# Kernel optimization log

Hardware: AMD Instinct MI355X
Metric: run time of the kernel (lower is better)

Reference implementation:

```python
import jax, jax.numpy as jnp
import numpy as np

B, T, D_IN = 512, 128, 256
H1, H2 = 1024, 1024
LABEL_DIM = 3


def _lstm_layer(x, W, U, b):
    """Run one keras-LSTMCell layer over x: [T, B, D_in] -> [T, B, H].

    Keras gate order is (i, f, g, o); c' = f*c + i*tanh(g); h = o*tanh(c').
    """
    H = U.shape[0]
    batch = x.shape[1]

    def step(carry, xt):
        h, c = carry
        z = xt @ W + h @ U + b  # [B, 4H]
        i, f, g, o = jnp.split(z, 4, axis=-1)
        i = jax.nn.sigmoid(i)
        f = jax.nn.sigmoid(f)
        g = jnp.tanh(g)
        o = jax.nn.sigmoid(o)
        c_new = f * c + i * g
        h_new = o * jnp.tanh(c_new)
        return (h_new, c_new), h_new

    init = (jnp.zeros((batch, H), x.dtype), jnp.zeros((batch, H), x.dtype))
    _, hs = jax.lax.scan(step, init, x)
    return hs  # [T, B, H]


def setup_inputs() -> dict:
    key = jax.random.key(0)
    ks = jax.random.split(key, 10)
    chars = jax.random.normal(ks[0], (B, T, D_IN), dtype=jnp.float32)
    # sequence lengths in [1, T] so sequence_length - 1 is a valid index
    sequence_length = jax.random.randint(ks[1], (B,), 1, T + 1)
    s = 0.05
    W1 = jax.random.normal(ks[2], (D_IN, 4 * H1), dtype=jnp.float32) * s
    U1 = jax.random.normal(ks[3], (H1, 4 * H1), dtype=jnp.float32) * s
    b1 = jnp.zeros((4 * H1,), dtype=jnp.float32)
    W2 = jax.random.normal(ks[4], (H1, 4 * H2), dtype=jnp.float32) * s
    U2 = jax.random.normal(ks[5], (H2, 4 * H2), dtype=jnp.float32) * s
    b2 = jnp.zeros((4 * H2,), dtype=jnp.float32)
    Wd = jax.random.normal(ks[6], (H2, LABEL_DIM), dtype=jnp.float32) * s
    bd = jnp.zeros((LABEL_DIM,), dtype=jnp.float32)
    return {"chars": chars, "sequence_length": sequence_length,
            "W1": W1, "U1": U1, "b1": b1,
            "W2": W2, "U2": U2, "b2": b2,
            "Wd": Wd, "bd": bd}


def reference(chars, sequence_length, W1, U1, b1, W2, U2, b2, Wd, bd):
    # chars: [B, T, 256] -> time-major [T, B, 256]
    x = jnp.transpose(chars, (1, 0, 2))
    x = _lstm_layer(x, W1, U1, b1)          # [T, B, H1]
    x = _lstm_layer(x, W2, U2, b2)          # [T, B, H2]
    # gather the hidden state at the last valid timestep of each sequence
    batch = chars.shape[0]
    hidden = x[sequence_length - 1, jnp.arange(batch)]  # [B, H2]
    return jax.nn.relu(hidden @ Wd + bd)    # [B, label_dim]
```

## Files before the change

### kernel.cpp

```cpp
#include <hip/hip_runtime.h>
#include <hip/hip_bf16.h>


typedef __hip_bfloat16 bf16;
typedef __attribute__((ext_vector_type(8))) short bfrag8;
typedef __attribute__((ext_vector_type(4))) float accf4;

#define BATCH 512
#define TSTEPS 128
#define DIN 256
#define H 1024
#define NG 4096

__device__ __forceinline__ float sigm(float x) { return 1.0f / (1.0f + __expf(-x)); }
__device__ __forceinline__ float tanh_f(float x) {
    float a = fabsf(x);
    float e = __expf(-2.0f * a);
    float t = (1.0f - e) / (1.0f + e);
    return x < 0.0f ? -t : t;
}
__device__ __forceinline__ unsigned short bfr16(float x) {
    bf16 h = __float2bfloat16(x);
    return *(unsigned short*)&h;
}
__device__ __forceinline__ void gll16(const void* g, void* l) {
    __builtin_amdgcn_global_load_lds(
        (const __attribute__((address_space(1))) unsigned int*)g,
        (__attribute__((address_space(3))) unsigned int*)l, 16, 0, 0);
}

__global__ void k_repack(const float* __restrict__ W, const float* __restrict__ U,
                         bf16* __restrict__ Bp, int KIN)
{
    __shared__ float tile[128][65];
    int kt = blockIdx.x, nt = blockIdx.y;
    int lane = threadIdx.x;
    int n = nt * 64 + lane;
    int orig = ((n >> 4) & 3) * 1024 + (n >> 7) * 32 + ((n >> 6) & 1) * 16 + (n & 15);
    for (int j = 0; j < 128; ++j) {
        int k = kt * 128 + j;
        tile[j][lane] = (k < KIN) ? W[(size_t)k * NG + orig]
                                  : U[(size_t)(k - KIN) * NG + orig];
    }
    __syncthreads();
    for (int u = 0; u < 16; ++u) {
        int cid = u * 64 + lane;
        int nloc = cid >> 4;
        int pos = cid & 15;
        int nn = nt * 64 + nloc;
        int kc = pos ^ (nn & 7);
        alignas(16) unsigned short pk[8];
        #pragma unroll
        for (int jj = 0; jj < 8; ++jj) pk[jj] = bfr16(tile[kc * 8 + jj][nloc]);
        *(int4*)(Bp + ((size_t)kt * NG + nn) * 128 + pos * 8) = *(int4*)pk;
    }
}

struct StepJob {
    const float* Xf;
    const bf16* A0;
    const bf16* A1;
    const bf16* Bp;
    const float* bias;
    float* C;
    bf16* Hout;
    float* hidden;
    const int* seqlen;
    int xstride;
    int ksplit;
    int KT;
    int t;
};

__global__ __launch_bounds__(256, 2) void k_step(StepJob j0, StepJob j1)
{
    __shared__ __align__(16) bf16 Alds[64 * 128];
    __shared__ __align__(16) bf16 Blds[128 * 128];

    const StepJob jb = (blockIdx.x >> 8) ? j1 : j0;
    int bi = blockIdx.x & 255;
    int tid = threadIdx.x;
    int wv = tid >> 6, lane = tid & 63;
    int ntile = bi & 31;
    int b0 = (bi >> 5) * 64;
    int n0 = ntile * 128;
    int mw = (wv & 1) * 32;
    int nw = (wv >> 1) * 64;
    int c = lane & 15, q = lane >> 4;

    const accf4 zero4 = {0.f, 0.f, 0.f, 0.f};
    accf4 acc[2][4];
    #pragma unroll
    for (int i = 0; i < 2; ++i)
        #pragma unroll
        for (int j = 0; j < 4; ++j) acc[i][j] = zero4;

    for (int kt = 0; kt < jb.KT; ++kt) {
        int k0 = kt << 7;
        if (jb.Xf && k0 < jb.ksplit) {
            #pragma unroll
            for (int uu = 0; uu < 4; ++uu) {
                int u = uu * 256 + tid;
                int r = u >> 4;
                int pos = u & 15;
                int kc = pos ^ (r & 7);
                const float* src = jb.Xf + (size_t)(b0 + r) * jb.xstride + k0 + kc * 8;
                float4 va = *(const float4*)src;
                float4 vb = *(const float4*)(src + 4);
                alignas(16) unsigned short pk[8];
                pk[0] = bfr16(va.x); pk[1] = bfr16(va.y);
                pk[2] = bfr16(va.z); pk[3] = bfr16(va.w);
                pk[4] = bfr16(vb.x); pk[5] = bfr16(vb.y);
                pk[6] = bfr16(vb.z); pk[7] = bfr16(vb.w);
                *(int4*)((char*)Alds + u * 16) = *(int4*)pk;
            }
        } else {
            const bf16* Asrc; int kk0;
            if (k0 < jb.ksplit) { Asrc = jb.A0; kk0 = k0; }
            else                { Asrc = jb.A1; kk0 = k0 - jb.ksplit; }
            #pragma unroll
            for (int cc = 0; cc < 4; ++cc) {
                int ob = wv * 4096 + cc * 1024;
                int o = ob + lane * 16;
                int r = o >> 8;
                const char* g = (const char*)Asrc + (size_t)(b0 + r) * (H * 2) + kk0 * 2 + (o & 255);
                gll16(g, (char*)Alds + ob);
            }
        }
        const char* Bg = (const char*)jb.Bp + ((size_t)kt * NG + n0) * 256;
        #pragma unroll
        for (int cc = 0; cc < 8; ++cc) {
            int ob = wv * 8192 + cc * 1024;
            gll16(Bg + ob + lane * 16, (char*)Blds + ob);
        }
        __syncthreads();
        #pragma unroll
        for (int kk = 0; kk < 128; kk += 32) {
            int kc = (kk >> 3) + q;
            int ra = mw + c;
            int pa = (kc ^ (ra & 7)) << 3;
            bfrag8 af0 = *(const bfrag8*)(Alds + ra * 128 + pa);
            bfrag8 af1 = *(const bfrag8*)(Alds + (ra + 16) * 128 + pa);
            #pragma unroll
            for (int nt = 0; nt < 4; ++nt) {
                int nn = nw + nt * 16 + c;
                bfrag8 bfv = *(const bfrag8*)(Blds + nn * 128 + ((kc ^ (nn & 7)) << 3));
                acc[0][nt] = __builtin_amdgcn_mfma_f32_16x16x32_bf16(af0, bfv, acc[0][nt], 0, 0, 0);
                acc[1][nt] = __builtin_amdgcn_mfma_f32_16x16x32_bf16(af1, bfv, acc[1][nt], 0, 0, 0);
            }
        }
        __syncthreads();
    }

    int hcol = ntile * 32 + (wv >> 1) * 16 + c;
    float bi_ = jb.bias[hcol],         bf_ = jb.bias[H + hcol];
    float bg_ = jb.bias[2 * H + hcol], bo_ = jb.bias[3 * H + hcol];
    int seg = hcol & ~127;
    int kc_ = (hcol & 127) >> 3;
    int jl = hcol & 7;
    #pragma unroll
    for (int mt = 0; mt < 2; ++mt) {
        #pragma unroll
        for (int reg = 0; reg < 4; ++reg) {
            int b = b0 + mw + mt * 16 + q * 4 + reg;
            float ig = sigm(acc[mt][0][reg] + bi_);
            float fg = sigm(acc[mt][1][reg] + bf_);
            float gv = tanh_f(acc[mt][2][reg] + bg_);
            float og = sigm(acc[mt][3][reg] + bo_);
            size_t ci = (size_t)b * H + hcol;
            float cv = fg * jb.C[ci] + ig * gv;
            jb.C[ci] = cv;
            float h = og * tanh_f(cv);
            jb.Hout[(size_t)b * H + seg + ((kc_ ^ (b & 7)) << 3) + jl] = __float2bfloat16(h);
            if (jb.hidden) {
                if (jb.seqlen[b] - 1 == jb.t) jb.hidden[ci] = h;
            }
        }
    }
}

__global__ void k_final(const float* __restrict__ hidden, const float* __restrict__ Wd,
                        const float* __restrict__ bd, float* __restrict__ out)
{
    int b = blockIdx.x;
    int l = threadIdx.x;
    float p0 = 0.f, p1 = 0.f, p2 = 0.f;
    for (int jj = l; jj < H; jj += 64) {
        float hv = hidden[(size_t)b * H + jj];
        p0 += hv * Wd[jj * 3 + 0];
        p1 += hv * Wd[jj * 3 + 1];
        p2 += hv * Wd[jj * 3 + 2];
    }
    #pragma unroll
    for (int off = 32; off > 0; off >>= 1) {
        p0 += __shfl_down(p0, off);
        p1 += __shfl_down(p1, off);
        p2 += __shfl_down(p2, off);
    }
    if (l == 0) {
        out[b * 3 + 0] = fmaxf(p0 + bd[0], 0.f);
        out[b * 3 + 1] = fmaxf(p1 + bd[1], 0.f);
        out[b * 3 + 2] = fmaxf(p2 + bd[2], 0.f);
    }
}

extern "C" void kernel_launch(void* const* d_in, const int* in_sizes, int n_in,
                              void* d_out, int out_size, void* d_ws, size_t ws_size,
                              hipStream_t stream)
{
    const float* chars = (const float*)d_in[0];
    const int* seqlen  = (const int*)d_in[1];
    const float* W1 = (const float*)d_in[2];
    const float* U1 = (const float*)d_in[3];
    const float* b1 = (const float*)d_in[4];
    const float* W2 = (const float*)d_in[5];
    const float* U2 = (const float*)d_in[6];
    const float* b2 = (const float*)d_in[7];
    const float* Wd = (const float*)d_in[8];
    const float* bd = (const float*)d_in[9];
    float* out = (float*)d_out;

    char* ws = (char*)d_ws;
    size_t off = 0;
    bf16* Bp1 = (bf16*)(ws + off); off += (size_t)10 * NG * 128 * 2;
    bf16* Bp2 = (bf16*)(ws + off); off += (size_t)16 * NG * 128 * 2;
    bf16* h1  = (bf16*)(ws + off); off += (size_t)2 * BATCH * H * 2;
    bf16* h2  = (bf16*)(ws + off); off += (size_t)2 * BATCH * H * 2;
    float* c1 = (float*)(ws + off); off += (size_t)BATCH * H * 4;
    float* c2 = (float*)(ws + off); off += (size_t)BATCH * H * 4;
    float* hidden = (float*)(ws + off); off += (size_t)BATCH * H * 4;
    if (ws_size < off) return;

    hipMemsetAsync(h1, 0, (size_t)2 * BATCH * H * 2, stream);
    hipMemsetAsync(h2, 0, (size_t)2 * BATCH * H * 2, stream);
    hipMemsetAsync(c1, 0, (size_t)BATCH * H * 4, stream);
    hipMemsetAsync(c2, 0, (size_t)BATCH * H * 4, stream);

    k_repack<<<dim3(10, 64), 64, 0, stream>>>(W1, U1, Bp1, 256);
    k_repack<<<dim3(16, 64), 64, 0, stream>>>(W2, U2, Bp2, 1024);

    const size_t HS = (size_t)BATCH * H;

    auto mkL1 = [&](int s) {
        StepJob J;
        J.Xf = chars + (size_t)s * DIN;  J.xstride = TSTEPS * DIN;
        J.A0 = nullptr;
        J.A1 = h1 + (size_t)((s + 1) & 1) * HS;
        J.Bp = Bp1; J.bias = b1; J.C = c1;
        J.Hout = h1 + (size_t)(s & 1) * HS;
        J.hidden = nullptr; J.seqlen = nullptr;
        J.ksplit = 256; J.KT = 10; J.t = s;
        return J;
    };
    auto mkL2 = [&](int s) {
        StepJob J;
        J.Xf = nullptr; J.xstride = 0;
        J.A0 = h1 + (size_t)(s & 1) * HS;
        J.A1 = h2 + (size_t)((s + 1) & 1) * HS;
        J.Bp = Bp2; J.bias = b2; J.C = c2;
        J.Hout = h2 + (size_t)(s & 1) * HS;
        J.hidden = hidden; J.seqlen = seqlen;
        J.ksplit = 1024; J.KT = 16; J.t = s;
        return J;
    };

    StepJob first = mkL1(0);
    k_step<<<256, 256, 0, stream>>>(first, first);
    for (int t = 0; t < TSTEPS - 1; ++t) {
        k_step<<<512, 256, 0, stream>>>(mkL2(t), mkL1(t + 1));
    }
    StepJob last = mkL2(TSTEPS - 1);
    k_step<<<256, 256, 0, stream>>>(last, last);
    k_final<<<512, 64, 0, stream>>>(hidden, Wd, bd, out);
}
```

Before: 3.660 ms.

## Replace per-step launches with persistent kernel using per-row-group atomic counters

```diff
diff --git a/kernel.cpp b/kernel.cpp
--- a/kernel.cpp
+++ b/kernel.cpp
@@ -56,126 +56,164 @@
     }
 }
 
-struct StepJob {
-    const float* Xf;
-    const bf16* A0;
-    const bf16* A1;
-    const bf16* Bp;
-    const float* bias;
-    float* C;
-    bf16* Hout;
-    float* hidden;
-    const int* seqlen;
-    int xstride;
-    int ksplit;
-    int KT;
-    int t;
+struct PP {
+    const float* chars; const int* seqlen;
+    const bf16* Bp1; const bf16* Bp2;
+    const float* b1; const float* b2;
+    bf16* h1; bf16* h2; float* hidden;
+    int* cnt1; int* cnt2;
 };
 
-__global__ __launch_bounds__(256, 2) void k_step(StepJob j0, StepJob j1)
+__global__ __launch_bounds__(256, 2) void k_persist(PP P)
 {
     __shared__ __align__(16) bf16 Alds[64 * 128];
     __shared__ __align__(16) bf16 Blds[128 * 128];
 
-    const StepJob jb = (blockIdx.x >> 8) ? j1 : j0;
-    int bi = blockIdx.x & 255;
-    int tid = threadIdx.x;
-    int wv = tid >> 6, lane = tid & 63;
-    int ntile = bi & 31;
-    int b0 = (bi >> 5) * 64;
-    int n0 = ntile * 128;
-    int mw = (wv & 1) * 32;
-    int nw = (wv >> 1) * 64;
-    int c = lane & 15, q = lane >> 4;
-
-    const accf4 zero4 = {0.f, 0.f, 0.f, 0.f};
-    accf4 acc[2][4];
+    const int bid = blockIdx.x;
+    const int job = bid >> 8;
+    const int bi = bid & 255;
+    const int tid = threadIdx.x;
+    const int wv = tid >> 6, lane = tid & 63;
+    const int ntile = bi & 31, rg = bi >> 5;
+    const int b0 = rg * 64, n0 = ntile * 128;
+    const int mw = (wv & 1) * 32, nw = (wv >> 1) * 64;
+    const int c = lane & 15, q = lane >> 4;
+
+    const bf16* Bp = job ? P.Bp2 : P.Bp1;
+    const float* bias = job ? P.b2 : P.b1;
+    const int KT = job ? 16 : 10;
+    const int ksplit = job ? 1024 : 256;
+    const size_t HS = (size_t)BATCH * H;
+
+    const int hcol = ntile * 32 + (wv >> 1) * 16 + c;
+    const float bi_ = bias[hcol],         bf_ = bias[H + hcol];
+    const float bg_ = bias[2 * H + hcol], bo_ = bias[3 * H + hcol];
+    const int seg = hcol & ~127;
+    const int kc_ = (hcol & 127) >> 3;
+    const int jl = hcol & 7;
+    int houti[8]; int hidi[8]; int sl[8]; float cellv[8];
     #pragma unroll
-    for (int i = 0; i < 2; ++i)
-        #pragma unroll
-        for (int j = 0; j < 4; ++j) acc[i][j] = zero4;
-
-    for (int kt = 0; kt < jb.KT; ++kt) {
-        int k0 = kt << 7;
-        if (jb.Xf && k0 < jb.ksplit) {
-            #pragma unroll
-            for (int uu = 0; uu < 4; ++uu) {
-                int u = uu * 256 + tid;
-                int r = u >> 4;
-                int pos = u & 15;
-                int kc = pos ^ (r & 7);
-                const float* src = jb.Xf + (size_t)(b0 + r) * jb.xstride + k0 + kc * 8;
-                float4 va = *(const float4*)src;
-                float4 vb = *(const float4*)(src + 4);
-                alignas(16) unsigned short pk[8];
-                pk[0] = bfr16(va.x); pk[1] = bfr16(va.y);
-                pk[2] = bfr16(va.z); pk[3] = bfr16(va.w);
-                pk[4] = bfr16(vb.x); pk[5] = bfr16(vb.y);
-                pk[6] = bfr16(vb.z); pk[7] = bfr16(vb.w);
-                *(int4*)((char*)Alds + u * 16) = *(int4*)pk;
-            }
-        } else {
-            const bf16* Asrc; int kk0;
-            if (k0 < jb.ksplit) { Asrc = jb.A0; kk0 = k0; }
-            else                { Asrc = jb.A1; kk0 = k0 - jb.ksplit; }
-            #pragma unroll
-            for (int cc = 0; cc < 4; ++cc) {
-                int ob = wv * 4096 + cc * 1024;
-                int o = ob + lane * 16;
-                int r = o >> 8;
-                const char* g = (const char*)Asrc + (size_t)(b0 + r) * (H * 2) + kk0 * 2 + (o & 255);
-                gll16(g, (char*)Alds + ob);
-            }
-        }
-        const char* Bg = (const char*)jb.Bp + ((size_t)kt * NG + n0) * 256;
+    for (int u = 0; u < 8; ++u) {
+        int b = b0 + mw + (u >> 2) * 16 + q * 4 + (u & 3);
+        houti[u] = b * H + seg + (((kc_ ^ (b & 7))) << 3) + jl;
+        hidi[u] = b * H + hcol;
+        sl[u] = job ? (P.seqlen[b] - 1) : -1;
+        cellv[u] = 0.f;
+    }
+
+    int* cme = (job ? P.cnt2 : P.cnt1) + rg * 16;
+    int* cn1 = P.cnt1 + rg * 16;
+    int* cn2 = P.cnt2 + rg * 16;
+
+    auto stageChars = [&](int t_, int k0) {
+        #pragma unroll
+        for (int uu = 0; uu < 4; ++uu) {
+            int u = uu * 256 + tid;
+            int r = u >> 4;
+            int pos = u & 15;
+            int kc = pos ^ (r & 7);
+            const float* src = P.chars + (size_t)(b0 + r) * (TSTEPS * DIN)
+                             + (size_t)t_ * DIN + k0 + kc * 8;
+            float4 va = *(const float4*)src;
+            float4 vb = *(const float4*)(src + 4);
+            alignas(16) unsigned short pk[8];
+            pk[0] = bfr16(va.x); pk[1] = bfr16(va.y);
+            pk[2] = bfr16(va.z); pk[3] = bfr16(va.w);
+            pk[4] = bfr16(vb.x); pk[5] = bfr16(vb.y);
+            pk[6] = bfr16(vb.z); pk[7] = bfr16(vb.w);
+            *(int4*)((char*)Alds + u * 16) = *(int4*)pk;
+        }
+    };
+    auto stageH = [&](const bf16* Asrc, int kk0) {
+        #pragma unroll
+        for (int cc = 0; cc < 4; ++cc) {
+            int ob = wv * 4096 + cc * 1024;
+            int o = ob + lane * 16;
+            int r = o >> 8;
+            const char* g = (const char*)Asrc + (size_t)(b0 + r) * (H * 2)
+                          + kk0 * 2 + (o & 255);
+            gll16(g, (char*)Alds + ob);
+        }
+    };
+    auto stageB = [&](int kt) {
+        const char* Bg = (const char*)Bp + ((size_t)kt * NG + n0) * 256;
         #pragma unroll
         for (int cc = 0; cc < 8; ++cc) {
             int ob = wv * 8192 + cc * 1024;
             gll16(Bg + ob + lane * 16, (char*)Blds + ob);
         }
+    };
+
+    for (int t = 0; t < TSTEPS; ++t) {
+        const bf16* A0 = job ? (P.h1 + (size_t)(t & 1) * HS) : nullptr;
+        const bf16* A1 = (job ? P.h2 : P.h1) + (size_t)((t + 1) & 1) * HS;
+        bf16* Hout = (job ? P.h2 : P.h1) + (size_t)(t & 1) * HS;
+
+        stageB(0);
+        if (!job) stageChars(t, 0);
+
+        int n1 = job ? 32 * (t + 1) : 32 * t;
+        int n2 = job ? 32 * t       : 32 * (t - 1);
+        if (tid == 0) {
+            while (__hip_atomic_load(cn1, __ATOMIC_RELAXED, __HIP_MEMORY_SCOPE_AGENT) < n1 ||
+                   __hip_atomic_load(cn2, __ATOMIC_RELAXED, __HIP_MEMORY_SCOPE_AGENT) < n2)
+                __builtin_amdgcn_s_sleep(8);
+        }
         __syncthreads();
-        #pragma unroll
-        for (int kk = 0; kk < 128; kk += 32) {
-            int kc = (kk >> 3) + q;
-            int ra = mw + c;
-            int pa = (kc ^ (ra & 7)) << 3;
-            bfrag8 af0 = *(const bfrag8*)(Alds + ra * 128 + pa);
-            bfrag8 af1 = *(const bfrag8*)(Alds + (ra + 16) * 128 + pa);
+        __threadfence();
+        if (job) stageH(A0, 0);
+
+        accf4 acc[2][4];
+        #pragma unroll
+        for (int i = 0; i < 2; ++i)
             #pragma unroll
-            for (int nt = 0; nt < 4; ++nt) {
-                int nn = nw + nt * 16 + c;
-                bfrag8 bfv = *(const bfrag8*)(Blds + nn * 128 + ((kc ^ (nn & 7)) << 3));
-                acc[0][nt] = __builtin_amdgcn_mfma_f32_16x16x32_bf16(af0, bfv, acc[0][nt], 0, 0, 0);
-                acc[1][nt] = __builtin_amdgcn_mfma_f32_16x16x32_bf16(af1, bfv, acc[1][nt], 0, 0, 0);
+            for (int jz = 0; jz < 4; ++jz) acc[i][jz] = accf4{0.f, 0.f, 0.f, 0.f};
+
+        for (int kt = 0; kt < KT; ++kt) {
+            if (kt > 0) {
+                int k0 = kt << 7;
+                if (!job && k0 < ksplit) stageChars(t, k0);
+                else if (k0 < ksplit)    stageH(A0, k0);
+                else                     stageH(A1, k0 - ksplit);
+                stageB(kt);
             }
-        }
-        __syncthreads();
-    }
-
-    int hcol = ntile * 32 + (wv >> 1) * 16 + c;
-    float bi_ = jb.bias[hcol],         bf_ = jb.bias[H + hcol];
-    float bg_ = jb.bias[2 * H + hcol], bo_ = jb.bias[3 * H + hcol];
-    int seg = hcol & ~127;
-    int kc_ = (hcol & 127) >> 3;
-    int jl = hcol & 7;
-    #pragma unroll
-    for (int mt = 0; mt < 2; ++mt) {
-        #pragma unroll
-        for (int reg = 0; reg < 4; ++reg) {
-            int b = b0 + mw + mt * 16 + q * 4 + reg;
+            __syncthreads();
+            #pragma unroll
+            for (int kk = 0; kk < 128; kk += 32) {
+                int kc = (kk >> 3) + q;
+                int ra = mw + c;
+                int pa = (kc ^ (ra & 7)) << 3;
+                bfrag8 af0 = *(const bfrag8*)(Alds + ra * 128 + pa);
+                bfrag8 af1 = *(const bfrag8*)(Alds + (ra + 16) * 128 + pa);
+                #pragma unroll
+                for (int nt = 0; nt < 4; ++nt) {
+                    int nn = nw + nt * 16 + c;
+                    bfrag8 bfv = *(const bfrag8*)(Blds + nn * 128 + ((kc ^ (nn & 7)) << 3));
+                    acc[0][nt] = __builtin_amdgcn_mfma_f32_16x16x32_bf16(af0, bfv, acc[0][nt], 0, 0, 0);
+                    acc[1][nt] = __builtin_amdgcn_mfma_f32_16x16x32_bf16(af1, bfv, acc[1][nt], 0, 0, 0);
+                }
+            }
+            __syncthreads();
+        }
+
+        #pragma unroll
+        for (int u = 0; u < 8; ++u) {
+            int mt = u >> 2, reg = u & 3;
             float ig = sigm(acc[mt][0][reg] + bi_);
             float fg = sigm(acc[mt][1][reg] + bf_);
             float gv = tanh_f(acc[mt][2][reg] + bg_);
             float og = sigm(acc[mt][3][reg] + bo_);
-            size_t ci = (size_t)b * H + hcol;
-            float cv = fg * jb.C[ci] + ig * gv;
-            jb.C[ci] = cv;
+            float cv = fg * cellv[u] + ig * gv;
+            cellv[u] = cv;
             float h = og * tanh_f(cv);
-            jb.Hout[(size_t)b * H + seg + ((kc_ ^ (b & 7)) << 3) + jl] = __float2bfloat16(h);
-            if (jb.hidden) {
-                if (jb.seqlen[b] - 1 == jb.t) jb.hidden[ci] = h;
-            }
-        }
+            Hout[houti[u]] = __float2bfloat16(h);
+            if (job && sl[u] == t) P.hidden[hidi[u]] = h;
+        }
+
+        __threadfence();
+        __syncthreads();
+        if (tid == 0)
+            __hip_atomic_fetch_add(cme, 1, __ATOMIC_RELEASE, __HIP_MEMORY_SCOPE_AGENT);
     }
 }
 
@@ -226,50 +264,24 @@
     bf16* Bp2 = (bf16*)(ws + off); off += (size_t)16 * NG * 128 * 2;
     bf16* h1  = (bf16*)(ws + off); off += (size_t)2 * BATCH * H * 2;
     bf16* h2  = (bf16*)(ws + off); off += (size_t)2 * BATCH * H * 2;
-    float* c1 = (float*)(ws + off); off += (size_t)BATCH * H * 4;
-    float* c2 = (float*)(ws + off); off += (size_t)BATCH * H * 4;
     float* hidden = (float*)(ws + off); off += (size_t)BATCH * H * 4;
+    int* cnt1 = (int*)(ws + off); off += 8 * 16 * 4;
+    int* cnt2 = (int*)(ws + off); off += 8 * 16 * 4;
     if (ws_size < off) return;
 
     hipMemsetAsync(h1, 0, (size_t)2 * BATCH * H * 2, stream);
     hipMemsetAsync(h2, 0, (size_t)2 * BATCH * H * 2, stream);
-    hipMemsetAsync(c1, 0, (size_t)BATCH * H * 4, stream);
-    hipMemsetAsync(c2, 0, (size_t)BATCH * H * 4, stream);
+    hipMemsetAsync(cnt1, 0, 2 * 8 * 16 * 4, stream);
 
     k_repack<<<dim3(10, 64), 64, 0, stream>>>(W1, U1, Bp1, 256);
     k_repack<<<dim3(16, 64), 64, 0, stream>>>(W2, U2, Bp2, 1024);
 
-    const size_t HS = (size_t)BATCH * H;
-
-    auto mkL1 = [&](int s) {
-        StepJob J;
-        J.Xf = chars + (size_t)s * DIN;  J.xstride = TSTEPS * DIN;
-        J.A0 = nullptr;
-        J.A1 = h1 + (size_t)((s + 1) & 1) * HS;
-        J.Bp = Bp1; J.bias = b1; J.C = c1;
-        J.Hout = h1 + (size_t)(s & 1) * HS;
-        J.hidden = nullptr; J.seqlen = nullptr;
-        J.ksplit = 256; J.KT = 10; J.t = s;
-        return J;
-    };
-    auto mkL2 = [&](int s) {
-        StepJob J;
-        J.Xf = nullptr; J.xstride = 0;
-        J.A0 = h1 + (size_t)(s & 1) * HS;
-        J.A1 = h2 + (size_t)((s + 1) & 1) * HS;
-        J.Bp = Bp2; J.bias = b2; J.C = c2;
-        J.Hout = h2 + (size_t)(s & 1) * HS;
-        J.hidden = hidden; J.seqlen = seqlen;
-        J.ksplit = 1024; J.KT = 16; J.t = s;
-        return J;
-    };
-
-    StepJob first = mkL1(0);
-    k_step<<<256, 256, 0, stream>>>(first, first);
-    for (int t = 0; t < TSTEPS - 1; ++t) {
-        k_step<<<512, 256, 0, stream>>>(mkL2(t), mkL1(t + 1));
-    }
-    StepJob last = mkL2(TSTEPS - 1);
-    k_step<<<256, 256, 0, stream>>>(last, last);
+    PP P;
+    P.chars = chars; P.seqlen = seqlen;
+    P.Bp1 = Bp1; P.Bp2 = Bp2; P.b1 = b1; P.b2 = b2;
+    P.h1 = h1; P.h2 = h2; P.hidden = hidden;
+    P.cnt1 = cnt1; P.cnt2 = cnt2;
+
+    k_persist<<<512, 256, 0, stream>>>(P);
     k_final<<<512, 64, 0, stream>>>(hidden, Wd, bd, out);
 }
```

After: 14.41 ms. 3.94x slower.
